# Kernel tuning notes

Hardware: AMD Instinct MI355X
Metric: run time of the kernel (lower is better)

Reference implementation:

```python
import jax, jax.numpy as jnp
import numpy as np

B, T, C, HS = 256, 256, 384, 64

def setup_inputs() -> dict:
    key = jax.random.key(0)
    ks = jax.random.split(key, 7)
    return {
        "x": jax.random.normal(ks[0], (B, T, C), dtype=jnp.float32),
        "Wq": jax.random.normal(ks[1], (C, HS), dtype=jnp.float32) * (C ** -0.5),
        "bq": jax.random.normal(ks[2], (HS,), dtype=jnp.float32) * 0.02,
        "Wk": jax.random.normal(ks[3], (C, HS), dtype=jnp.float32) * (C ** -0.5),
        "bk": jax.random.normal(ks[4], (HS,), dtype=jnp.float32) * 0.02,
        "Wv": jax.random.normal(ks[5], (C, HS), dtype=jnp.float32) * (C ** -0.5),
        "bv": jax.random.normal(ks[6], (HS,), dtype=jnp.float32) * 0.02,
    }

def reference(x, Wq, bq, Wk, bk, Wv, bv):
    # single-head causal self-attention (eval mode: dropout is identity)
    T_ = x.shape[1]
    q = x @ Wq + bq          # [B, T, HS]
    k = x @ Wk + bk          # [B, T, HS]
    v = x @ Wv + bv          # [B, T, HS]
    scale = k.shape[-1] ** -0.5
    att = jnp.einsum("btd,bsd->bts", q, k) * scale   # [B, T, T]
    causal = jnp.tril(jnp.ones((T_, T_), dtype=bool))  # tril buffer
    att = jnp.where(causal, att, -jnp.inf)             # mask future positions
    att = jax.nn.softmax(att, axis=-1)
    return jnp.einsum("bts,bsd->btd", att, v)          # [B, T, HS]
```

## Files before the change

### kernel.cpp

```cpp
#include <hip/hip_runtime.h>
#include <hip/hip_bf16.h>

#define BB 256
#define TT 256
#define CC 384
#define HSS 64

typedef __bf16 bf16_t;
typedef bf16_t bf16x8 __attribute__((ext_vector_type(8)));
typedef bf16_t bf16x4 __attribute__((ext_vector_type(4)));
typedef float f32x4 __attribute__((ext_vector_type(4)));

__device__ __forceinline__ f32x4 mfma16(bf16x8 a, bf16x8 b, f32x4 c) {
    return __builtin_amdgcn_mfma_f32_16x16x32_bf16(a, b, c, 0, 0, 0);
}

__device__ __forceinline__ bf16x8 cvt8(float4 a, float4 b) {
    bf16x8 r;
    r[0] = (bf16_t)a.x; r[1] = (bf16_t)a.y; r[2] = (bf16_t)a.z; r[3] = (bf16_t)a.w;
    r[4] = (bf16_t)b.x; r[5] = (bf16_t)b.y; r[6] = (bf16_t)b.z; r[7] = (bf16_t)b.w;
    return r;
}

typedef __attribute__((address_space(3))) unsigned int lds_uint_t;
typedef const __attribute__((address_space(1))) unsigned int glb_uint_t;
__device__ __forceinline__ void async_cp16(const void* g, void* lds_uniform) {
    __builtin_amdgcn_global_load_lds((glb_uint_t*)g, (lds_uint_t*)lds_uniform, 16, 0, 0);
}

__global__ void prep_w(const float* __restrict__ Wq, const float* __restrict__ Wk,
                       const float* __restrict__ Wv, bf16_t* __restrict__ WtG) {
    int idx = blockIdx.x * 256 + threadIdx.x;
    if (idx >= 192 * 384) return;
    int n = idx / 384, k = idx % 384;
    const float* W = (n < 64) ? Wq : (n < 128) ? Wk : Wv;
    float val = W[k * 64 + (n & 63)];
    int kc = k >> 7, kin = k & 127;
    int c = kin >> 3, e = k & 7;
    int pc = c ^ (n & 15);
    WtG[kc * 24576 + n * 128 + pc * 8 + e] = (bf16_t)val;
}

__global__ __attribute__((amdgpu_flat_work_group_size(512, 512),
                          amdgpu_waves_per_eu(2, 2)))
void head_fused(
    const float* __restrict__ x, const bf16_t* __restrict__ WtG,
    const float* __restrict__ bq, const float* __restrict__ bk, const float* __restrict__ bv,
    float* __restrict__ out) {

    __shared__ bf16_t Wl[24576];
    __shared__ uint4 Ksw[2048];
    __shared__ uint4 Vsw[2048];
    __shared__ __align__(16) bf16_t Pb[8 * 640];

    int b = blockIdx.x, tid = threadIdx.x;
    int w = tid >> 6, l = tid & 63, lr = l & 15, lq = l >> 4;
    int Mt[2] = {w, 15 - w};

    float bqv[4], bkv[4], bvv[4];
#pragma unroll
    for (int nt = 0; nt < 4; nt++) {
        bqv[nt] = bq[nt * 16 + lr];
        bkv[nt] = bk[nt * 16 + lr];
        bvv[nt] = bv[nt * 16 + lr];
    }

    const float* xr[2];
    xr[0] = x + ((size_t)b * TT + Mt[0] * 16 + lr) * CC;
    xr[1] = x + ((size_t)b * TT + Mt[1] * 16 + lr) * CC;

    f32x4 acc[2][12];
#pragma unroll
    for (int m = 0; m < 2; m++)
#pragma unroll
        for (int i = 0; i < 12; i++) acc[m][i] = (f32x4){0.f, 0.f, 0.f, 0.f};

    for (int kc = 0; kc < 3; kc++) {
        if (kc) __syncthreads();
        const bf16_t* src = WtG + kc * 24576;
#pragma unroll
        for (int j = 0; j < 6; j++) {
            int cbase = (j * 8 + w) * 64;
            async_cp16(src + (size_t)(cbase + l) * 8, Wl + (size_t)cbase * 8);
        }
        bf16x8 af[2][4];
#pragma unroll
        for (int m = 0; m < 2; m++) {
            const float* xp = xr[m] + kc * 128 + lq * 8;
#pragma unroll
            for (int t = 0; t < 4; t++) {
                float4 f0 = *(const float4*)(xp + t * 32);
                float4 f1 = *(const float4*)(xp + t * 32 + 4);
                af[m][t] = cvt8(f0, f1);
            }
        }
        __syncthreads();
#pragma unroll
        for (int nt = 0; nt < 12; nt++) {
            const bf16_t* wl = Wl + (size_t)(nt * 16 + lr) * 128;
#pragma unroll
            for (int t = 0; t < 4; t++) {
                int pc = (t * 4 + lq) ^ lr;
                bf16x8 bfrag = *(const bf16x8*)(wl + pc * 8);
                acc[0][nt] = mfma16(af[0][t], bfrag, acc[0][nt]);
                acc[1][nt] = mfma16(af[1][t], bfrag, acc[1][nt]);
            }
        }
    }

    bf16_t* KswB = (bf16_t*)Ksw;
    bf16_t* VswB = (bf16_t*)Vsw;
#pragma unroll
    for (int m = 0; m < 2; m++) {
#pragma unroll
        for (int nt = 4; nt < 8; nt++) {
            int d = (nt - 4) * 16 + lr;
#pragma unroll
            for (int r = 0; r < 4; r++) {
                int s = Mt[m] * 16 + lq * 4 + r;
                KswB[s * 64 + ((d >> 3) ^ (s & 7)) * 8 + (d & 7)] =
                    (bf16_t)(acc[m][nt][r] + bkv[nt - 4]);
            }
        }
#pragma unroll
        for (int nt = 8; nt < 12; nt++) {
            int d = (nt - 8) * 16 + lr;
            int t0 = Mt[m] * 16 + lq * 4;
            int c = t0 >> 3;
            bf16x4 pk;
#pragma unroll
            for (int r = 0; r < 4; r++) pk[r] = (bf16_t)(acc[m][nt][r] + bvv[nt - 8]);
            *(bf16x4*)(VswB + d * 256 + ((c & ~7) | ((c ^ d) & 7)) * 8 + (t0 & 7)) = pk;
        }
    }
    __syncthreads();

    const float scale2 = 0.125f * 1.4426950408889634f;
    bf16_t* Pw = Pb + w * 640;

#pragma unroll
    for (int m = 0; m < 2; m++) {
        int R0 = Mt[m] * 16;
        int tg = R0 + lr;
        int ktm = Mt[m] >> 1;

        bf16x8 qf[2];
#pragma unroll
        for (int hh = 0; hh < 2; hh++) {
#pragma unroll
            for (int u = 0; u < 2; u++) {
                int nt = 2 * hh + u;
#pragma unroll
                for (int r = 0; r < 4; r++)
                    Pw[(lq * 4 + r) * 40 + u * 16 + lr] =
                        (bf16_t)(acc[m][nt][r] + bqv[nt]);
            }
            qf[hh] = *(const bf16x8*)(Pw + lr * 40 + lq * 8);
        }

        f32x4 oacc[4] = {};
        float sum = 0.f;
#pragma unroll
        for (int kt = 0; kt < 8; kt++) {
            if (kt <= ktm) {
#pragma unroll
                for (int u = 0; u < 2; u++) {
                    int nt = kt * 2 + u;
                    int s = nt * 16 + lr;
                    const uint4* krow = Ksw + s * 8;
                    bf16x8 k0 = __builtin_bit_cast(bf16x8, krow[lq ^ (s & 7)]);
                    bf16x8 k1 = __builtin_bit_cast(bf16x8, krow[(4 + lq) ^ (s & 7)]);
                    f32x4 a = {0.f, 0.f, 0.f, 0.f};
                    a = mfma16(k0, qf[0], a);
                    a = mfma16(k1, qf[1], a);
                    bf16x4 pk;
#pragma unroll
                    for (int r = 0; r < 4; r++) {
                        int sg = nt * 16 + lq * 4 + r;
                        float p = (sg <= tg) ? exp2f(a[r] * scale2) : 0.f;
                        sum += p;
                        pk[r] = (bf16_t)p;
                    }
                    *(bf16x4*)(Pw + lr * 40 + u * 16 + lq * 4) = pk;
                }
                bf16x8 pf = *(const bf16x8*)(Pw + lr * 40 + lq * 8);
#pragma unroll
                for (int dt = 0; dt < 4; dt++) {
                    int d = dt * 16 + lr;
                    int cc = kt * 4 + lq;
                    bf16x8 vf = __builtin_bit_cast(bf16x8,
                        Vsw[d * 32 + ((cc & ~7) | ((cc ^ d) & 7))]);
                    oacc[dt] = mfma16(vf, pf, oacc[dt]);
                }
            }
        }

        sum += __shfl_xor(sum, 16);
        sum += __shfl_xor(sum, 32);
        float inv = 1.0f / sum;

        float* orow = out + ((size_t)b * TT + R0 + lr) * HSS;
#pragma unroll
        for (int dt = 0; dt < 4; dt++) {
            float4 o;
            o.x = oacc[dt][0] * inv;
            o.y = oacc[dt][1] * inv;
            o.z = oacc[dt][2] * inv;
            o.w = oacc[dt][3] * inv;
            *(float4*)(orow + dt * 16 + lq * 4) = o;
        }
    }
}

extern "C" void kernel_launch(void* const* d_in, const int* in_sizes, int n_in,
                              void* d_out, int out_size, void* d_ws, size_t ws_size,
                              hipStream_t stream) {
    const float* x  = (const float*)d_in[0];
    const float* Wq = (const float*)d_in[1];
    const float* bq = (const float*)d_in[2];
    const float* Wk = (const float*)d_in[3];
    const float* bk = (const float*)d_in[4];
    const float* Wv = (const float*)d_in[5];
    const float* bv = (const float*)d_in[6];
    float* out = (float*)d_out;

    bf16_t* WtG = (bf16_t*)d_ws;

    prep_w<<<288, 256, 0, stream>>>(Wq, Wk, Wv, WtG);
    head_fused<<<BB, 512, 0, stream>>>(x, WtG, bq, bk, bv, out);
}
```

Measured before the change: 178.8 us.

## Double-buffer weight chunks and prefetch x in the QKV projection loop

Measured after the change: 177.2 us. Within noise of the previous version (-0.9%).

```diff
diff --git a/kernel.cpp b/kernel.cpp
--- a/kernel.cpp
+++ b/kernel.cpp
@@ -35,10 +35,10 @@
     int n = idx / 384, k = idx % 384;
     const float* W = (n < 64) ? Wq : (n < 128) ? Wk : Wv;
     float val = W[k * 64 + (n & 63)];
-    int kc = k >> 7, kin = k & 127;
+    int kc = k >> 6, kin = k & 63;
     int c = kin >> 3, e = k & 7;
-    int pc = c ^ (n & 15);
-    WtG[kc * 24576 + n * 128 + pc * 8 + e] = (bf16_t)val;
+    int pc = c ^ (n & 7);
+    WtG[kc * 12288 + n * 64 + pc * 8 + e] = (bf16_t)val;
 }
 
 __global__ __attribute__((amdgpu_flat_work_group_size(512, 512),
@@ -48,7 +48,7 @@
     const float* __restrict__ bq, const float* __restrict__ bk, const float* __restrict__ bv,
     float* __restrict__ out) {
 
-    __shared__ bf16_t Wl[24576];
+    __shared__ bf16_t Wl[2][12288];
     __shared__ uint4 Ksw[2048];
     __shared__ uint4 Vsw[2048];
     __shared__ __align__(16) bf16_t Pb[8 * 640];
@@ -75,38 +75,60 @@
 #pragma unroll
         for (int i = 0; i < 12; i++) acc[m][i] = (f32x4){0.f, 0.f, 0.f, 0.f};
 
-    for (int kc = 0; kc < 3; kc++) {
-        if (kc) __syncthreads();
-        const bf16_t* src = WtG + kc * 24576;
-#pragma unroll
-        for (int j = 0; j < 6; j++) {
-            int cbase = (j * 8 + w) * 64;
-            async_cp16(src + (size_t)(cbase + l) * 8, Wl + (size_t)cbase * 8);
-        }
-        bf16x8 af[2][4];
-#pragma unroll
-        for (int m = 0; m < 2; m++) {
-            const float* xp = xr[m] + kc * 128 + lq * 8;
-#pragma unroll
-            for (int t = 0; t < 4; t++) {
-                float4 f0 = *(const float4*)(xp + t * 32);
-                float4 f1 = *(const float4*)(xp + t * 32 + 4);
-                af[m][t] = cvt8(f0, f1);
-            }
-        }
+    float4 xf[2][2][2];
+
+#define DMA_CHUNK(kc, buf)                                                   \
+    {                                                                        \
+        const bf16_t* _src = WtG + (kc) * 12288;                             \
+        _Pragma("unroll")                                                    \
+        for (int j = 0; j < 3; j++) {                                        \
+            int cbase = (j * 8 + w) * 64;   \
+            async_cp16(_src + (size_t)(cbase + l) * 8,                       \
+                       &Wl[buf][(size_t)cbase * 8]);                         \
+        }                                                                    \
+    }
+#define LOAD_X(kc)                                                           \
+    {                                                                        \
+        _Pragma("unroll")                                                    \
+        for (int m = 0; m < 2; m++)                                          \
+            _Pragma("unroll")                                                \
+            for (int t = 0; t < 2; t++) {                                    \
+                const float* xp = xr[m] + (kc) * 64 + t * 32 + lq * 8;       \
+                xf[m][t][0] = *(const float4*)xp;                            \
+                xf[m][t][1] = *(const float4*)(xp + 4);                      \
+            }                                                                \
+    }
+
+    DMA_CHUNK(0, 0);
+    LOAD_X(0);
+
+#pragma unroll
+    for (int kc = 0; kc < 6; kc++) {
         __syncthreads();
+        bf16x8 af[2][2];
+#pragma unroll
+        for (int m = 0; m < 2; m++)
+#pragma unroll
+            for (int t = 0; t < 2; t++) af[m][t] = cvt8(xf[m][t][0], xf[m][t][1]);
+        if (kc < 5) {
+            DMA_CHUNK(kc + 1, (kc + 1) & 1);
+            LOAD_X(kc + 1);
+        }
+        const bf16_t* buf = Wl[kc & 1];
 #pragma unroll
         for (int nt = 0; nt < 12; nt++) {
-            const bf16_t* wl = Wl + (size_t)(nt * 16 + lr) * 128;
-#pragma unroll
-            for (int t = 0; t < 4; t++) {
-                int pc = (t * 4 + lq) ^ lr;
+            const bf16_t* wl = buf + (size_t)(nt * 16 + lr) * 64;
+#pragma unroll
+            for (int t = 0; t < 2; t++) {
+                int pc = (t * 4 + lq) ^ (lr & 7);
                 bf16x8 bfrag = *(const bf16x8*)(wl + pc * 8);
                 acc[0][nt] = mfma16(af[0][t], bfrag, acc[0][nt]);
                 acc[1][nt] = mfma16(af[1][t], bfrag, acc[1][nt]);
             }
         }
     }
+#undef DMA_CHUNK
+#undef LOAD_X
 
     bf16_t* KswB = (bf16_t*)Ksw;
     bf16_t* VswB = (bf16_t*)Vsw;
```
